# Kernel tuning notes

Hardware: AMD Instinct MI355X
Metric: run time of the kernel (lower is better)

The kernel has to match this reference:

```python
import jax, jax.numpy as jnp
import numpy as np

B, S, D = 8, 1024, 768
H, HD = 12, 64
FF = 3072
EPS = 1e-5


def layernorm(x, w, b):
    mu = jnp.mean(x, axis=-1, keepdims=True)
    var = jnp.mean(jnp.square(x - mu), axis=-1, keepdims=True)
    return (x - mu) / jnp.sqrt(var + EPS) * w + b


def setup_inputs() -> dict:
    key = jax.random.key(0)
    ks = jax.random.split(key, 16)
    s_in = 1.0 / np.sqrt(D)
    s_p = 1.0 / np.sqrt(H * HD)
    s_ff = 1.0 / np.sqrt(FF)
    return {
        "x": jax.random.normal(ks[0], (B, S, D), dtype=jnp.float32),
        "ln1_w": jnp.ones((D,), jnp.float32),
        "ln1_b": jnp.zeros((D,), jnp.float32),
        "Wq": jax.random.uniform(ks[1], (H, D, HD), jnp.float32, -s_in, s_in),
        "bq": jax.random.uniform(ks[2], (H, HD), jnp.float32, -s_in, s_in),
        "Wk": jax.random.uniform(ks[3], (H, D, HD), jnp.float32, -s_in, s_in),
        "bk": jax.random.uniform(ks[4], (H, HD), jnp.float32, -s_in, s_in),
        "Wv": jax.random.uniform(ks[5], (H, D, HD), jnp.float32, -s_in, s_in),
        "bv": jax.random.uniform(ks[6], (H, HD), jnp.float32, -s_in, s_in),
        "Wp": jax.random.uniform(ks[7], (H * HD, D), jnp.float32, -s_p, s_p),
        "bp": jax.random.uniform(ks[8], (D,), jnp.float32, -s_p, s_p),
        "ln2_w": jnp.ones((D,), jnp.float32),
        "ln2_b": jnp.zeros((D,), jnp.float32),
        "W1": jax.random.uniform(ks[9], (D, FF), jnp.float32, -s_in, s_in),
        "b1": jax.random.uniform(ks[10], (FF,), jnp.float32, -s_in, s_in),
        "W2": jax.random.uniform(ks[11], (FF, D), jnp.float32, -s_ff, s_ff),
        "b2": jax.random.uniform(ks[12], (D,), jnp.float32, -s_ff, s_ff),
    }


def reference(x, ln1_w, ln1_b, Wq, bq, Wk, bk, Wv, bv, Wp, bp,
              ln2_w, ln2_b, W1, b1, W2, b2):
    gelu = lambda t: jax.nn.gelu(t, approximate=False)
    # --- multi-head self attention (NOTE: original never applies scale) ---
    y = layernorm(x, ln1_w, ln1_b)                       # [B,S,D]
    q = jnp.einsum('bsd,hde->bhse', y, Wq) + bq[:, None, :][None]
    k = jnp.einsum('bsd,hde->bhse', y, Wk) + bk[:, None, :][None]
    v = jnp.einsum('bsd,hde->bhse', y, Wv) + bv[:, None, :][None]
    attn = jax.nn.softmax(jnp.einsum('bhse,bhte->bhst', q, k), axis=-1)
    out = jnp.einsum('bhst,bhte->bhse', attn, v)         # [B,H,S,HD]
    out = out.transpose(0, 2, 1, 3).reshape(x.shape[0], x.shape[1], -1)  # concat heads
    y = gelu(out @ Wp + bp)                              # projection + GELU
    x = x + y                                            # residual 1
    # --- MLP block ---
    h = layernorm(x, ln2_w, ln2_b)
    h = gelu(h @ W1 + b1)
    h = gelu(h @ W2 + b2)
    return x + h                                         # residual 2
```

## Files before the change

### kernel.cpp

```cpp
#include <hip/hip_runtime.h>
#include <hip/hip_bf16.h>
#include <math.h>

#define BB 8
#define SS 1024
#define DD 768
#define HH 12
#define HDD 64
#define FFF 3072
#define NROW (BB*SS)
#define QKVN (3*DD)

typedef __hip_bfloat16 bf16;
typedef __bf16 bf16x8 __attribute__((ext_vector_type(8)));
typedef float floatx4 __attribute__((ext_vector_type(4)));

__device__ __forceinline__ float gelu_fast(float x) {
    float u = x * fmaf(0.07135481627f, x * x, 1.595769122f);
    float e = __expf(u);
    return x * e * __builtin_amdgcn_rcpf(e + 1.0f);
}

__device__ __forceinline__ unsigned short f2bfbits(float f) {
    bf16 h = __float2bfloat16(f);
    return __builtin_bit_cast(unsigned short, h);
}

__device__ __forceinline__ void gload16(const void* g, void* l) {
    __builtin_amdgcn_global_load_lds(
        (const __attribute__((address_space(1))) unsigned int*)g,
        (__attribute__((address_space(3))) unsigned int*)l, 16, 0, 0);
}

template<typename T>
__global__ __launch_bounds__(256) void ln_kernel(const T* __restrict__ x,
                                                 const float* __restrict__ w,
                                                 const float* __restrict__ b,
                                                 bf16* __restrict__ y) {
    int wave = threadIdx.x >> 6, lane = threadIdx.x & 63;
    int row = blockIdx.x * 4 + wave;
    const T* xr = x + (size_t)row * DD;
    bf16* yr = y + (size_t)row * DD;

    float v[12];
    #pragma unroll
    for (int s = 0; s < 3; s++) {
        int base = s * 256 + lane * 4;
        if constexpr (__is_same(T, float)) {
            float4 f = *(const float4*)(xr + base);
            v[s*4+0] = f.x; v[s*4+1] = f.y; v[s*4+2] = f.z; v[s*4+3] = f.w;
        } else {
            ushort4 u = *(const ushort4*)(xr + base);
            v[s*4+0] = __bfloat162float(__builtin_bit_cast(bf16, u.x));
            v[s*4+1] = __bfloat162float(__builtin_bit_cast(bf16, u.y));
            v[s*4+2] = __bfloat162float(__builtin_bit_cast(bf16, u.z));
            v[s*4+3] = __bfloat162float(__builtin_bit_cast(bf16, u.w));
        }
    }
    float sum = 0.f, sq = 0.f;
    #pragma unroll
    for (int i = 0; i < 12; i++) { sum += v[i]; sq += v[i] * v[i]; }
    #pragma unroll
    for (int off = 1; off < 64; off <<= 1) {
        sum += __shfl_xor(sum, off, 64);
        sq  += __shfl_xor(sq,  off, 64);
    }
    float mu  = sum * (1.0f / DD);
    float var = sq * (1.0f / DD) - mu * mu;
    float inv = rsqrtf(var + 1e-5f);

    #pragma unroll
    for (int s = 0; s < 3; s++) {
        int base = s * 256 + lane * 4;
        float4 wf = *(const float4*)(w + base);
        float4 bf = *(const float4*)(b + base);
        ushort4 o;
        o.x = f2bfbits((v[s*4+0] - mu) * inv * wf.x + bf.x);
        o.y = f2bfbits((v[s*4+1] - mu) * inv * wf.y + bf.y);
        o.z = f2bfbits((v[s*4+2] - mu) * inv * wf.z + bf.z);
        o.w = f2bfbits((v[s*4+3] - mu) * inv * wf.w + bf.w);
        *(ushort4*)(yr + base) = o;
    }
}

__global__ __launch_bounds__(256) void prep_kernel(
    const float* __restrict__ Wq, const float* __restrict__ Wk,
    const float* __restrict__ Wv, const float* __restrict__ Wp,
    const float* __restrict__ W1, const float* __restrict__ W2,
    const float* __restrict__ bq, const float* __restrict__ bk,
    const float* __restrict__ bv,
    bf16* __restrict__ Wqkvt, bf16* __restrict__ Wpt,
    bf16* __restrict__ W1t, bf16* __restrict__ W2t, float* __restrict__ bqkv)
{
    int id = blockIdx.x;
    if (id >= 6912) {
        int i = (id - 6912) * 256 + threadIdx.x;
        if (i < DD) { bqkv[i] = bq[i]; bqkv[DD + i] = bk[i]; bqkv[2*DD + i] = bv[i]; }
        return;
    }
    const float* src; bf16* dst; int K, N, hmode, local;
    if (id < 1728)      { K = DD;  N = DD;  hmode = 1; local = id % 576;
                          src = (id < 576) ? Wq : (id < 1152 ? Wk : Wv);
                          dst = Wqkvt + (size_t)(id / 576) * DD * DD; }
    else if (id < 2304) { K = DD;  N = DD;  hmode = 0; local = id - 1728; src = Wp; dst = Wpt; }
    else if (id < 4608) { K = DD;  N = FFF; hmode = 0; local = id - 2304; src = W1; dst = W1t; }
    else                { K = FFF; N = DD;  hmode = 0; local = id - 4608; src = W2; dst = W2t; }
    int ktiles = K / 32;
    int k0 = (local % ktiles) * 32, n0 = (local / ktiles) * 32;
    __shared__ float t[32][33];
    int tx = threadIdx.x & 31, ty4 = threadIdx.x >> 5;
    #pragma unroll
    for (int i = 0; i < 4; i++) {
        int k = k0 + ty4 * 4 + i;
        int n = n0 + tx;
        size_t si = hmode ? ((size_t)(n >> 6) * K * 64 + (size_t)k * 64 + (n & 63))
                          : ((size_t)k * N + n);
        t[ty4 * 4 + i][tx] = src[si];
    }
    __syncthreads();
    #pragma unroll
    for (int i = 0; i < 4; i++) {
        int n = n0 + ty4 * 4 + i;
        int k = k0 + tx;
        dst[(size_t)n * K + k] = __float2bfloat16(t[tx][ty4 * 4 + i]);
    }
}

template<int MT, int KH, int DEPTH>
__global__ __launch_bounds__(256) void mfma_gemm(
    const bf16* __restrict__ A, const bf16* __restrict__ Bt,
    const float* __restrict__ bias, const float* __restrict__ residf,
    const bf16* __restrict__ residb, void* __restrict__ Cout,
    int M, int N, int K, int act, int out_bf16, int nx, int py,
    int qkvmode, bf16* __restrict__ qhg, bf16* __restrict__ khg, bf16* __restrict__ vtg)
{
    constexpr int MFRAG = MT / 32;
    constexpr int ACH = MT * 4;
    constexpr int A_LOADS = ACH * KH / 256;
    constexpr int B_LOADS = 2 * KH;
    constexpr int LOADS = A_LOADS + B_LOADS;
    constexpr unsigned ABYTES = KH * MT * 32 * 2;
    constexpr unsigned BBYTES = KH * 128 * 32 * 2;
    static_assert(DEPTH == 2 || (DEPTH == 3 && LOADS == 4), "vmcnt literal fixed at 4");
    __shared__ bf16 As[DEPTH][KH * MT * 32];
    __shared__ bf16 Bs[DEPTH][KH * 128 * 32];
    int tid = threadIdx.x;
    int id = blockIdx.x;
    int xcd = id & 7, slot = id >> 3;
    int rp = slot % py, ct = slot / py;
    int row0 = (xcd * py + rp) * MT, col0 = ct * 128;
    int wave = tid >> 6, lane = tid & 63;
    int wm = (wave >> 1) * (MT / 2), wn = (wave & 1) * 64;
    int l16 = lane & 15, quad = lane >> 4;

    const bf16* pA[A_LOADS]; unsigned ldA[A_LOADS];
    #pragma unroll
    for (int i = 0; i < A_LOADS; i++) {
        int c = tid + i * 256;
        int half = c / ACH, rem = c % ACH;
        int r = rem >> 2, pos = rem & 3;
        int ksw = half * 32 + ((pos ^ ((r >> 1) & 3)) << 3);
        pA[i] = A + (size_t)(row0 + r) * K + ksw;
        ldA[i] = (unsigned)c * 16u;
    }
    const bf16* pB[B_LOADS]; unsigned ldB[B_LOADS];
    #pragma unroll
    for (int i = 0; i < B_LOADS; i++) {
        int c = tid + i * 256;
        int half = c >> 9, rem = c & 511;
        int r = rem >> 2, pos = rem & 3;
        int ksw = half * 32 + ((pos ^ ((r >> 1) & 3)) << 3);
        pB[i] = Bt + (size_t)(col0 + r) * K + ksw;
        ldB[i] = (unsigned)c * 16u;
    }
    char* lbaseA = (char*)&As[0][0];
    char* lbaseB = (char*)&Bs[0][0];

    auto stage = [&](int k0, int buf) {
        char* dA = lbaseA + (unsigned)buf * ABYTES;
        char* dB = lbaseB + (unsigned)buf * BBYTES;
        #pragma unroll
        for (int i = 0; i < A_LOADS; i++) gload16(pA[i] + k0, dA + ldA[i]);
        #pragma unroll
        for (int i = 0; i < B_LOADS; i++) gload16(pB[i] + k0, dB + ldB[i]);
    };

    unsigned roA[KH][MFRAG], roB[KH][4];
    #pragma unroll
    for (int s = 0; s < KH; s++) {
        #pragma unroll
        for (int mt = 0; mt < MFRAG; mt++) {
            int r = wm + mt * 16 + l16;
            int pos = quad ^ ((r >> 1) & 3);
            roA[s][mt] = (unsigned)(s * MT * 32 + r * 32 + pos * 8) * 2u;
        }
        #pragma unroll
        for (int nt = 0; nt < 4; nt++) {
            int r = wn + nt * 16 + l16;
            int pos = quad ^ ((r >> 1) & 3);
            roB[s][nt] = (unsigned)(s * 4096 + r * 32 + pos * 8) * 2u;
        }
    }

    floatx4 acc[MFRAG][4] = {};

    auto compute = [&](int cur) {
        const char* bA = lbaseA + (unsigned)cur * ABYTES;
        const char* bB = lbaseB + (unsigned)cur * BBYTES;
        #pragma unroll
        for (int s = 0; s < KH; s++) {
            bf16x8 af[MFRAG], bfr[4];
            #pragma unroll
            for (int mt = 0; mt < MFRAG; mt++)
                af[mt] = *(const bf16x8*)(bA + roA[s][mt]);
            #pragma unroll
            for (int nt = 0; nt < 4; nt++)
                bfr[nt] = *(const bf16x8*)(bB + roB[s][nt]);
            #pragma unroll
            for (int mt = 0; mt < MFRAG; mt++)
                #pragma unroll
                for (int nt = 0; nt < 4; nt++)
                    acc[mt][nt] = __builtin_amdgcn_mfma_f32_16x16x32_bf16(
                        af[mt], bfr[nt], acc[mt][nt], 0, 0, 0);
        }
    };

    if constexpr (DEPTH == 3) {
        int T = K / (32 * KH);
        stage(0, 0);
        if (T > 1) stage(32 * KH, 1);
        for (int t = 0; t < T; t++) {
            if (t == T - 1) { asm volatile("s_waitcnt vmcnt(0)" ::: "memory"); }
            else            { asm volatile("s_waitcnt vmcnt(4)" ::: "memory"); }
            __builtin_amdgcn_s_barrier();
            if (t + 2 < T) stage((t + 2) * (32 * KH), (t + 2) % 3);
            compute(t % 3);
        }
    } else {
        stage(0, 0);
        int cur = 0;
        for (int k0 = 0; k0 < K; k0 += 32 * KH) {
            __syncthreads();
            if (k0 + 32 * KH < K) stage(k0 + 32 * KH, cur ^ 1);
            compute(cur);
            cur ^= 1;
        }
    }

    if (qkvmode) {
        #pragma unroll
        for (int mt = 0; mt < MFRAG; mt++) {
            int rbase = row0 + wm + mt * 16 + quad * 4;
            int bq_ = rbase >> 10, sb = rbase & 1023;
            #pragma unroll
            for (int nt = 0; nt < 4; nt++) {
                int col = col0 + wn + nt * 16 + l16;
                float bcol = bias[col];
                if (col < DD) {
                    int hh = col >> 6, e = col & 63;
                    bf16* base = qhg + (((size_t)bq_ * HH + hh) * SS + sb) * 64 + e;
                    #pragma unroll
                    for (int r = 0; r < 4; r++)
                        base[(size_t)r * 64] = __float2bfloat16(acc[mt][nt][r] + bcol);
                } else if (col < 2 * DD) {
                    int cc = col - DD, hh = cc >> 6, e = cc & 63;
                    bf16* base = khg + (((size_t)bq_ * HH + hh) * SS) * 64;
                    #pragma unroll
                    for (int r = 0; r < 4; r++) {
                        int s = sb + r;
                        int pos = (((e >> 3) ^ (s & 7)) << 3) | (e & 7);
                        base[(size_t)s * 64 + pos] = __float2bfloat16(acc[mt][nt][r] + bcol);
                    }
                } else {
                    int cc = col - 2 * DD, hh = cc >> 6, e = cc & 63;
                    int c_t = sb >> 3;
                    int sc = (c_t & ~7) | ((c_t & 7) ^ (e & 7));
                    size_t off = (((size_t)bq_ * HH + hh) * 64 + e) * SS + sc * 8 + (sb & 7);
                    ushort4 pk;
                    pk.x = f2bfbits(acc[mt][nt][0] + bcol);
                    pk.y = f2bfbits(acc[mt][nt][1] + bcol);
                    pk.z = f2bfbits(acc[mt][nt][2] + bcol);
                    pk.w = f2bfbits(acc[mt][nt][3] + bcol);
                    *(ushort4*)&vtg[off] = pk;
                }
            }
        }
        return;
    }

    #pragma unroll
    for (int mt = 0; mt < MFRAG; mt++) {
        int rbase = row0 + wm + mt * 16 + quad * 4;
        #pragma unroll
        for (int nt = 0; nt < 4; nt++) {
            int col = col0 + wn + nt * 16 + l16;
            float bcol = bias[col];
            #pragma unroll
            for (int r = 0; r < 4; r++) {
                int row = rbase + r;
                float v = acc[mt][nt][r] + bcol;
                if (act) v = gelu_fast(v);
                if (residf) v += residf[(size_t)row * N + col];
                if (residb) v += __bfloat162float(residb[(size_t)row * N + col]);
                if (out_bf16) ((bf16*)Cout)[(size_t)row * N + col] = __float2bfloat16(v);
                else          ((float*)Cout)[(size_t)row * N + col] = v;
            }
        }
    }
}

__global__ __launch_bounds__(512) void gemm8(
    const bf16* __restrict__ A, const bf16* __restrict__ Bt,
    const float* __restrict__ bias, const bf16* __restrict__ residb,
    void* __restrict__ Cout, int N, int K, int act, int out_bf16, int py)
{
    __shared__ bf16 As[2][2][256 * 32];
    __shared__ bf16 Bs[2][2][128 * 32];
    int tid = threadIdx.x;
    int id = blockIdx.x;
    int xcd = id & 7, slot = id >> 3;
    int rp = slot % py, ct = slot / py;
    int row0 = (xcd * py + rp) * 256, col0 = ct * 128;
    int wave = tid >> 6, lane = tid & 63;
    int wm = (wave >> 1) * 64, wn = (wave & 1) * 64;
    int l16 = lane & 15, quad = lane >> 4;

    const bf16* pA[2]; unsigned ldA[2];
    #pragma unroll
    for (int i = 0; i < 2; i++) {
        int c = tid + i * 512;
        int r = c >> 2, pos = c & 3;
        pA[i] = A + (size_t)(row0 + r) * K + ((pos ^ ((r >> 1) & 3)) << 3);
        ldA[i] = (unsigned)c * 16u;
    }
    const bf16* pB; unsigned ldB;
    {
        int r = tid >> 2, pos = tid & 3;
        pB = Bt + (size_t)(col0 + r) * K + ((pos ^ ((r >> 1) & 3)) << 3);
        ldB = (unsigned)tid * 16u;
    }
    auto stage = [&](int kt, int buf, int s) {
        int kof = kt * 64 + s * 32;
        char* dA = (char*)&As[buf][s][0];
        char* dB = (char*)&Bs[buf][s][0];
        gload16(pA[0] + kof, dA + ldA[0]);
        gload16(pA[1] + kof, dA + ldA[1]);
        gload16(pB + kof, dB + ldB);
    };

    unsigned roA[4], roB[4];
    #pragma unroll
    for (int mt = 0; mt < 4; mt++) {
        int r = wm + mt * 16 + l16;
        int pos = quad ^ ((r >> 1) & 3);
        roA[mt] = (unsigned)(r * 32 + pos * 8) * 2u;
    }
    #pragma unroll
    for (int nt = 0; nt < 4; nt++) {
        int r = wn + nt * 16 + l16;
        int pos = quad ^ ((r >> 1) & 3);
        roB[nt] = (unsigned)(r * 32 + pos * 8) * 2u;
    }

    floatx4 acc[4][4] = {};
    int KT = K >> 6;

    stage(0, 0, 0);
    stage(0, 0, 1);

    for (int t = 0; t < KT; t++) {
        int cb = t & 1;
        #pragma unroll
        for (int s = 0; s < 2; s++) {
            if (s == 1 && t == KT - 1) { asm volatile("s_waitcnt vmcnt(0)" ::: "memory"); }
            else                       { asm volatile("s_waitcnt vmcnt(3)" ::: "memory"); }
            __builtin_amdgcn_s_barrier();
            const char* bA = (const char*)&As[cb][s][0];
            const char* bB = (const char*)&Bs[cb][s][0];
            bf16x8 af[4], bfr[4];
            #pragma unroll
            for (int mt = 0; mt < 4; mt++) af[mt] = *(const bf16x8*)(bA + roA[mt]);
            #pragma unroll
            for (int nt = 0; nt < 4; nt++) bfr[nt] = *(const bf16x8*)(bB + roB[nt]);
            if (t + 1 < KT) stage(t + 1, cb ^ 1, s);
            asm volatile("s_waitcnt lgkmcnt(0)" ::: "memory");
            __builtin_amdgcn_sched_barrier(0);
            __builtin_amdgcn_s_setprio(1);
            #pragma unroll
            for (int mt = 0; mt < 4; mt++)
                #pragma unroll
                for (int nt = 0; nt < 4; nt++)
                    acc[mt][nt] = __builtin_amdgcn_mfma_f32_16x16x32_bf16(
                        af[mt], bfr[nt], acc[mt][nt], 0, 0, 0);
            __builtin_amdgcn_s_setprio(0);
        }
    }

    #pragma unroll
    for (int mt = 0; mt < 4; mt++) {
        int rbase = row0 + wm + mt * 16 + quad * 4;
        #pragma unroll
        for (int nt = 0; nt < 4; nt++) {
            int col = col0 + wn + nt * 16 + l16;
            float bcol = bias[col];
            #pragma unroll
            for (int r = 0; r < 4; r++) {
                int row = rbase + r;
                float v = acc[mt][nt][r] + bcol;
                if (act) v = gelu_fast(v);
                if (residb) v += __bfloat162float(residb[(size_t)row * N + col]);
                if (out_bf16) ((bf16*)Cout)[(size_t)row * N + col] = __float2bfloat16(v);
                else          ((float*)Cout)[(size_t)row * N + col] = v;
            }
        }
    }
}

__global__ __launch_bounds__(256) void attn_mfma(
    const bf16* __restrict__ qh, const bf16* __restrict__ kh,
    const bf16* __restrict__ vT, bf16* __restrict__ ao)
{
    __shared__ bf16 Ks[2][64 * 64];
    __shared__ bf16 Vs[2][64 * 64];
    __shared__ bf16 Ps[128 * 64];

    int tid = threadIdx.x;
    int wave = tid >> 6, lane = tid & 63;
    int l16 = lane & 15, quad = lane >> 4;
    int id = blockIdx.x;
    int bh = (id & 7) * 12 + ((id >> 3) >> 3);
    int b = bh / HH, h = bh % HH;
    int s0 = ((id >> 3) & 7) * 128;
    int wm = wave * 32;

    const bf16* qbase = qh + ((size_t)bh * SS) * HDD;
    const bf16* kbase = kh + ((size_t)bh * SS) * HDD;
    const bf16* vbase = vT + ((size_t)bh * HDD) * SS;

    auto stage = [&](int t0, int buf) {
        #pragma unroll
        for (int i = 0; i < 2; i++) {
            int c = tid + i * 256;
            gload16(kbase + (size_t)t0 * 64 + c * 8, &Ks[buf][c * 8]);
            gload16(vbase + (size_t)(c >> 3) * SS + t0 + (c & 7) * 8, &Vs[buf][c * 8]);
        }
    };

    bf16x8 qf[2][2];
    #pragma unroll
    for (int mt = 0; mt < 2; mt++)
        #pragma unroll
        for (int ks = 0; ks < 2; ks++)
            qf[mt][ks] = *(const bf16x8*)(qbase +
                (size_t)(s0 + wm + mt * 16 + l16) * HDD + ks * 32 + quad * 8);

    floatx4 oaccT[4][2] = {};
    float lsum[2] = {};

    stage(0, 0);
    int cur = 0;
    for (int t0 = 0; t0 < SS; t0 += 64) {
        __syncthreads();
        if (t0 + 64 < SS) stage(t0 + 64, cur ^ 1);

        floatx4 st[4][2] = {};
        #pragma unroll
        for (int tt = 0; tt < 4; tt++) {
            int t = tt * 16 + l16;
            #pragma unroll
            for (int ks = 0; ks < 2; ks++) {
                int pos = (quad + 4 * ks) ^ (t & 7);
                bf16x8 kf = *(const bf16x8*)(&Ks[cur][t * 64 + pos * 8]);
                #pragma unroll
                for (int mt = 0; mt < 2; mt++)
                    st[tt][mt] = __builtin_amdgcn_mfma_f32_16x16x32_bf16(
                        kf, qf[mt][ks], st[tt][mt], 0, 0, 0);
            }
        }

        #pragma unroll
        for (int tt = 0; tt < 4; tt++)
            #pragma unroll
            for (int mt = 0; mt < 2; mt++) {
                float p0 = __expf(st[tt][mt][0]);
                float p1 = __expf(st[tt][mt][1]);
                float p2 = __expf(st[tt][mt][2]);
                float p3 = __expf(st[tt][mt][3]);
                lsum[mt] += (p0 + p1) + (p2 + p3);
                int m = wm + mt * 16 + l16;
                int c = tt * 2 + (quad >> 1);
                ushort4 pk;
                pk.x = f2bfbits(p0); pk.y = f2bfbits(p1);
                pk.z = f2bfbits(p2); pk.w = f2bfbits(p3);
                *(ushort4*)&Ps[m * 64 + ((c ^ (m & 7)) << 3) + (quad & 1) * 4] = pk;
            }

        #pragma unroll
        for (int ks = 0; ks < 2; ks++) {
            bf16x8 pf[2];
            #pragma unroll
            for (int mt = 0; mt < 2; mt++) {
                int m = wm + mt * 16 + l16;
                pf[mt] = *(const bf16x8*)(&Ps[m * 64 + (((quad + 4 * ks) ^ (m & 7)) << 3)]);
            }
            #pragma unroll
            for (int et = 0; et < 4; et++) {
                int e = et * 16 + l16;
                int vpos = (quad + 4 * ks) ^ (e & 7);
                bf16x8 vf = *(const bf16x8*)(&Vs[cur][e * 64 + vpos * 8]);
                #pragma unroll
                for (int mt = 0; mt < 2; mt++)
                    oaccT[et][mt] = __builtin_amdgcn_mfma_f32_16x16x32_bf16(
                        vf, pf[mt], oaccT[et][mt], 0, 0, 0);
            }
        }
        cur ^= 1;
    }

    float linv[2];
    #pragma unroll
    for (int mt = 0; mt < 2; mt++) {
        float l = lsum[mt];
        l += __shfl_xor(l, 16, 64);
        l += __shfl_xor(l, 32, 64);
        linv[mt] = __builtin_amdgcn_rcpf(l);
    }
    #pragma unroll
    for (int et = 0; et < 4; et++)
        #pragma unroll
        for (int mt = 0; mt < 2; mt++) {
            int m = wm + mt * 16 + l16;
            int c = et * 2 + (quad >> 1);
            ushort4 pk;
            pk.x = f2bfbits(oaccT[et][mt][0] * linv[mt]);
            pk.y = f2bfbits(oaccT[et][mt][1] * linv[mt]);
            pk.z = f2bfbits(oaccT[et][mt][2] * linv[mt]);
            pk.w = f2bfbits(oaccT[et][mt][3] * linv[mt]);
            *(ushort4*)&Ps[m * 64 + ((c ^ (m & 7)) << 3) + (quad & 1) * 4] = pk;
        }
    int mrow = wm + (lane >> 1);
    bf16* op = ao + ((size_t)b * SS + s0 + mrow) * DD + h * HDD;
    #pragma unroll
    for (int i = 0; i < 4; i++) {
        int j = (lane & 1) * 4 + i;
        bf16x8 v = *(const bf16x8*)&Ps[mrow * 64 + ((j ^ (mrow & 7)) << 3)];
        *(bf16x8*)&op[j * 8] = v;
    }
}

extern "C" void kernel_launch(void* const* d_in, const int* in_sizes, int n_in,
                              void* d_out, int out_size, void* d_ws, size_t ws_size,
                              hipStream_t stream)
{
    (void)in_sizes; (void)n_in; (void)out_size; (void)ws_size;
    const float* x    = (const float*)d_in[0];
    const float* ln1w = (const float*)d_in[1];
    const float* ln1b = (const float*)d_in[2];
    const float* Wq   = (const float*)d_in[3];
    const float* bq   = (const float*)d_in[4];
    const float* Wk   = (const float*)d_in[5];
    const float* bk   = (const float*)d_in[6];
    const float* Wv   = (const float*)d_in[7];
    const float* bv   = (const float*)d_in[8];
    const float* Wp   = (const float*)d_in[9];
    const float* bp   = (const float*)d_in[10];
    const float* ln2w = (const float*)d_in[11];
    const float* ln2b = (const float*)d_in[12];
    const float* W1   = (const float*)d_in[13];
    const float* b1   = (const float*)d_in[14];
    const float* W2   = (const float*)d_in[15];
    const float* b2   = (const float*)d_in[16];
    float* out = (float*)d_out;

    char* p = (char*)d_ws;
    auto alloc = [&](size_t bytes) { char* r = p; p += (bytes + 255) & ~255ull; return r; };
    bf16*  Wqkvt = (bf16*)alloc((size_t)QKVN * DD * 2);
    bf16*  Wpt   = (bf16*)alloc((size_t)DD * DD * 2);
    bf16*  W1t   = (bf16*)alloc((size_t)FFF * DD * 2);
    bf16*  W2t   = (bf16*)alloc((size_t)DD * FFF * 2);
    float* bqkv  = (float*)alloc((size_t)QKVN * 4);
    bf16*  yb    = (bf16*)alloc((size_t)NROW * DD * 2);
    bf16*  x1b   = (bf16*)alloc((size_t)NROW * DD * 2);
    char*  dynr  = alloc((size_t)NROW * DD * 2 + 3 * ((size_t)NROW * DD * 2));
    bf16*  aob   = (bf16*)dynr;
    bf16*  qhb   = (bf16*)(dynr + (size_t)NROW * DD * 2);
    bf16*  khb   = qhb + (size_t)NROW * DD;
    bf16*  vtb   = khb + (size_t)NROW * DD;
    bf16*  hb    = (bf16*)dynr;

    prep_kernel<<<6915, 256, 0, stream>>>(Wq, Wk, Wv, Wp, W1, W2, bq, bk, bv,
                                          Wqkvt, Wpt, W1t, W2t, bqkv);

    ln_kernel<float><<<NROW/4, 256, 0, stream>>>(x, ln1w, ln1b, yb);

    mfma_gemm<128,1,3><<<1152, 256, 0, stream>>>(
        yb, Wqkvt, bqkv, nullptr, nullptr, nullptr, NROW, QKVN, DD, 0, 0, 18, 8,
        1, qhb, khb, vtb);

    attn_mfma<<<dim3(BB*HH*(SS/128)), 256, 0, stream>>>(qhb, khb, vtb, aob);

    mfma_gemm<64,2,2><<<768, 256, 0, stream>>>(
        aob, Wpt, bp, x, nullptr, x1b, NROW, DD, DD, 1, 1, 6, 16,
        0, nullptr, nullptr, nullptr);

    ln_kernel<bf16><<<NROW/4, 256, 0, stream>>>(x1b, ln2w, ln2b, yb);

    gemm8<<<768, 512, 0, stream>>>(yb, W1t, b1, nullptr, hb, FFF, DD, 1, 1, 4);

    gemm8<<<192, 512, 0, stream>>>(hb, W2t, b2, x1b, out, DD, FFF, 1, 0, 4);
}
```

Measured before the change: 380.8 us.

## Deepen gemm8 LDS pipeline and route W2 GEMM through smaller-tile kernel

The 256x128 MLP GEMM kernel now keeps six half-K LDS stages, three loads in flight, and double-buffers register fragments. Each phase reads the next fragments while the MFMAs for the current ones run, which hides LDS and global latency better. The W2 down-projection now uses the 64-tile mfma_gemm with 768 blocks instead of gemm8 with 192, giving more parallelism across CUs. The cost is more LDS per block (144 KB) and more register pressure, which may reduce occupancy.

```diff
diff --git a/kernel.cpp b/kernel.cpp
--- a/kernel.cpp
+++ b/kernel.cpp
@@ -309,13 +309,13 @@
     }
 }
 
-__global__ __launch_bounds__(512) void gemm8(
+__global__ __launch_bounds__(512) void gemm8p(
     const bf16* __restrict__ A, const bf16* __restrict__ Bt,
     const float* __restrict__ bias, const bf16* __restrict__ residb,
     void* __restrict__ Cout, int N, int K, int act, int out_bf16, int py)
 {
-    __shared__ bf16 As[2][2][256 * 32];
-    __shared__ bf16 Bs[2][2][128 * 32];
+    __shared__ bf16 As[6][256 * 32];
+    __shared__ bf16 Bs[6][128 * 32];
     int tid = threadIdx.x;
     int id = blockIdx.x;
     int xcd = id & 7, slot = id >> 3;
@@ -339,10 +339,14 @@
         pB = Bt + (size_t)(col0 + r) * K + ((pos ^ ((r >> 1) & 3)) << 3);
         ldB = (unsigned)tid * 16u;
     }
-    auto stage = [&](int kt, int buf, int s) {
-        int kof = kt * 64 + s * 32;
-        char* dA = (char*)&As[buf][s][0];
-        char* dB = (char*)&Bs[buf][s][0];
+    char* lbA = (char*)&As[0][0];
+    char* lbB = (char*)&Bs[0][0];
+
+    auto stageR = [&](int r) {
+        int reg = ((r >> 1) % 3) * 2 + (r & 1);
+        char* dA = lbA + (unsigned)reg * 16384u;
+        char* dB = lbB + (unsigned)reg * 8192u;
+        int kof = r * 32;
         gload16(pA[0] + kof, dA + ldA[0]);
         gload16(pA[1] + kof, dA + ldA[1]);
         gload16(pB + kof, dB + ldB);
@@ -362,38 +366,54 @@
         roB[nt] = (unsigned)(r * 32 + pos * 8) * 2u;
     }
 
+    auto rdFrag = [&](int r, bf16x8 (&A8)[4], bf16x8 (&B8)[4]) {
+        int reg = ((r >> 1) % 3) * 2 + (r & 1);
+        const char* bA = lbA + (unsigned)reg * 16384u;
+        const char* bB = lbB + (unsigned)reg * 8192u;
+        #pragma unroll
+        for (int mt = 0; mt < 4; mt++) A8[mt] = *(const bf16x8*)(bA + roA[mt]);
+        #pragma unroll
+        for (int nt = 0; nt < 4; nt++) B8[nt] = *(const bf16x8*)(bB + roB[nt]);
+    };
+
     floatx4 acc[4][4] = {};
-    int KT = K >> 6;
-
-    stage(0, 0, 0);
-    stage(0, 0, 1);
-
-    for (int t = 0; t < KT; t++) {
-        int cb = t & 1;
-        #pragma unroll
-        for (int s = 0; s < 2; s++) {
-            if (s == 1 && t == KT - 1) { asm volatile("s_waitcnt vmcnt(0)" ::: "memory"); }
-            else                       { asm volatile("s_waitcnt vmcnt(3)" ::: "memory"); }
-            __builtin_amdgcn_s_barrier();
-            const char* bA = (const char*)&As[cb][s][0];
-            const char* bB = (const char*)&Bs[cb][s][0];
-            bf16x8 af[4], bfr[4];
-            #pragma unroll
-            for (int mt = 0; mt < 4; mt++) af[mt] = *(const bf16x8*)(bA + roA[mt]);
-            #pragma unroll
-            for (int nt = 0; nt < 4; nt++) bfr[nt] = *(const bf16x8*)(bB + roB[nt]);
-            if (t + 1 < KT) stage(t + 1, cb ^ 1, s);
-            asm volatile("s_waitcnt lgkmcnt(0)" ::: "memory");
-            __builtin_amdgcn_sched_barrier(0);
-            __builtin_amdgcn_s_setprio(1);
-            #pragma unroll
-            for (int mt = 0; mt < 4; mt++)
-                #pragma unroll
-                for (int nt = 0; nt < 4; nt++)
-                    acc[mt][nt] = __builtin_amdgcn_mfma_f32_16x16x32_bf16(
-                        af[mt], bfr[nt], acc[mt][nt], 0, 0, 0);
-            __builtin_amdgcn_s_setprio(0);
-        }
+    auto domfma = [&](bf16x8 (&A8)[4], bf16x8 (&B8)[4]) {
+        __builtin_amdgcn_s_setprio(1);
+        #pragma unroll
+        for (int mt = 0; mt < 4; mt++)
+            #pragma unroll
+            for (int nt = 0; nt < 4; nt++)
+                acc[mt][nt] = __builtin_amdgcn_mfma_f32_16x16x32_bf16(
+                    A8[mt], B8[nt], acc[mt][nt], 0, 0, 0);
+        __builtin_amdgcn_s_setprio(0);
+    };
+
+    int P = (K >> 6) * 2;
+    bf16x8 fA0[4], fB0[4], fA1[4], fB1[4];
+
+    stageR(0); stageR(1); stageR(2); stageR(3);
+    asm volatile("s_waitcnt vmcnt(9)" ::: "memory");
+    __builtin_amdgcn_s_barrier();
+    rdFrag(0, fA0, fB0);
+
+    auto phase = [&](int p, bf16x8 (&rA)[4], bf16x8 (&rB)[4],
+                     bf16x8 (&mA)[4], bf16x8 (&mB)[4]) {
+        int rem = P - 1 - p;
+        if (rem >= 3)      { asm volatile("s_waitcnt vmcnt(6)" ::: "memory"); }
+        else if (rem == 2) { asm volatile("s_waitcnt vmcnt(3)" ::: "memory"); }
+        else if (rem == 1) { asm volatile("s_waitcnt vmcnt(0)" ::: "memory"); }
+        __builtin_amdgcn_s_barrier();
+        if (rem >= 1) rdFrag(p + 1, rA, rB);
+        if (p + 4 < P) stageR(p + 4);
+        if (rem >= 1) { asm volatile("s_waitcnt lgkmcnt(8)" ::: "memory"); }
+        else          { asm volatile("s_waitcnt lgkmcnt(0)" ::: "memory"); }
+        __builtin_amdgcn_sched_barrier(0);
+        domfma(mA, mB);
+    };
+
+    for (int p = 0; p < P; p += 2) {
+        phase(p,     fA1, fB1, fA0, fB0);
+        phase(p + 1, fA0, fB0, fA1, fB1);
     }
 
     #pragma unroll
@@ -605,7 +625,9 @@
 
     ln_kernel<bf16><<<NROW/4, 256, 0, stream>>>(x1b, ln2w, ln2b, yb);
 
-    gemm8<<<768, 512, 0, stream>>>(yb, W1t, b1, nullptr, hb, FFF, DD, 1, 1, 4);
-
-    gemm8<<<192, 512, 0, stream>>>(hb, W2t, b2, x1b, out, DD, FFF, 1, 0, 4);
-}
+    gemm8p<<<768, 512, 0, stream>>>(yb, W1t, b1, nullptr, hb, FFF, DD, 1, 1, 4);
+
+    mfma_gemm<64,2,2><<<768, 256, 0, stream>>>(
+        hb, W2t, b2, nullptr, x1b, out, NROW, DD, FFF, 1, 0, 6, 16,
+        0, nullptr, nullptr, nullptr);
+}
```

Measured after the change: 372.6 us. 1.02x faster.
